# Performance work log

Hardware: AMD Instinct MI355X
Metric: run time of the kernel (lower is better)

Reference implementation:

```python
import jax, jax.numpy as jnp
import numpy as np

C = 256      # d_model
H = 8        # nhead
DF = 1024    # dim_feedforward
LE = 2048    # ego tokens
LA = 2048    # other-agent tokens
N_MATCH = 1024


def setup_inputs() -> dict:
    key = jax.random.key(0)
    ks = jax.random.split(key, 16)
    def rn(k, shape, s=0.02):
        return jax.random.normal(k, shape, dtype=jnp.float32) * s
    inp = {}
    inp['x_ego'] = jax.random.normal(ks[0], (LE, C), dtype=jnp.float32)
    inp['x_agent'] = jax.random.normal(ks[1], (LA, C), dtype=jnp.float32)
    # query_fusion MLP(2C -> C -> C -> C), torch Linear weight is (out, in)
    inp['Wf1'] = rn(ks[2], (C, 2 * C)); inp['bf1'] = jnp.zeros((C,), jnp.float32)
    inp['Wf2'] = rn(ks[3], (C, C));     inp['bf2'] = jnp.zeros((C,), jnp.float32)
    inp['Wf3'] = rn(ks[4], (C, C));     inp['bf3'] = jnp.zeros((C,), jnp.float32)
    # nn.MultiheadAttention packed in-proj and out-proj
    inp['Wqkv'] = rn(ks[5], (3 * C, C)); inp['bqkv'] = jnp.zeros((3 * C,), jnp.float32)
    inp['Wo'] = rn(ks[6], (C, C));       inp['bo'] = jnp.zeros((C,), jnp.float32)
    # FFN
    inp['W1'] = rn(ks[7], (DF, C)); inp['b1'] = jnp.zeros((DF,), jnp.float32)
    inp['W2'] = rn(ks[8], (C, DF)); inp['b2'] = jnp.zeros((C,), jnp.float32)
    # LayerNorms
    inp['g1'] = jnp.ones((C,), jnp.float32); inp['be1'] = jnp.zeros((C,), jnp.float32)
    inp['g2'] = jnp.ones((C,), jnp.float32); inp['be2'] = jnp.zeros((C,), jnp.float32)
    # unique 1D positions: first N_MATCH agent positions overlap ego, rest don't
    inp['pos_ego'] = jnp.arange(LE, dtype=jnp.int32)
    pa = np.concatenate([np.arange(N_MATCH), np.arange(LA - N_MATCH) + 10_000_000])
    inp['pos_agent'] = jnp.asarray(pa, dtype=jnp.int32)
    inp['n_remain'] = LA - N_MATCH  # static python int
    return inp


def _ln(t, g, b):
    m = t.mean(-1, keepdims=True)
    v = t.var(-1, keepdims=True)
    return (t - m) / jnp.sqrt(v + 1e-5) * g + b


def reference(x_ego, x_agent, Wf1, bf1, Wf2, bf2, Wf3, bf3, Wqkv, bqkv, Wo, bo,
              W1, b1, W2, b2, g1, be1, g2, be2, pos_ego, pos_agent, n_remain):
    # ---- position-keyed grouping / fuse (replaces the host-side dict loop) ----
    eq = pos_agent[:, None] == pos_ego[None, :]          # [La, Le]
    matched_e = eq.any(axis=0)                           # ego token has same-pos agent token
    agent_for_ego = jnp.argmax(eq, axis=0)               # [Le] matching agent index (valid where matched)
    fused_in = jnp.concatenate([x_ego, x_agent[agent_for_ego]], axis=-1)  # [Le, 2C]
    h = jax.nn.relu(fused_in @ Wf1.T + bf1)
    h = jax.nn.relu(h @ Wf2.T + bf2)
    fused = h @ Wf3.T + bf3                              # query_fusion MLP output [Le, C]
    ego_out = jnp.where(matched_e[:, None], fused, x_ego)
    # agent tokens with no ego match, in original agent order (fixed count n_remain)
    remain_idx = jnp.nonzero(~eq.any(axis=1), size=n_remain)[0]
    q = jnp.concatenate([ego_out, x_agent[remain_idx]], axis=0)[None]  # (1, Lq, C)
    kv = jnp.concatenate([x_ego, x_agent], axis=0)[None]               # (1, Lk, C)
    # ---- MultiheadAttention (batch_first, eval: dropout off) ----
    Wq, Wk, Wv = jnp.split(Wqkv, 3, axis=0)
    bq, bk, bv = jnp.split(bqkv, 3, axis=0)
    dh = C // H
    def heads(t, W, b):
        return (t @ W.T + b).reshape(1, -1, H, dh).transpose(0, 2, 1, 3)
    qh, kh, vh = heads(q, Wq, bq), heads(kv, Wk, bk), heads(kv, Wv, bv)
    scores = jnp.einsum('bhqd,bhkd->bhqk', qh, kh) / (float(dh) ** 0.5)
    attn = jax.nn.softmax(scores, axis=-1)
    o = jnp.einsum('bhqk,bhkd->bhqd', attn, vh).transpose(0, 2, 1, 3).reshape(1, -1, C)
    o = o @ Wo.T + bo
    # ---- residual + norm1 + FFN + residual + norm2 ----
    yq = _ln(q + o, g1, be1)
    ff = jax.nn.relu(yq @ W1.T + b1) @ W2.T + b2
    return _ln(yq + ff, g2, be2)
```

## Files before the change

kernel.cpp:

```cpp
#include <hip/hip_runtime.h>


#define LE 2048
#define LA 2048
#define CDIM 256
#define HN 8
#define DH 32
#define DFF 1024
#define NREM 1024
#define LQC 3072
#define LKC 4096
#define KSPLIT 8
#define NIT (LKC / KSPLIT / 64)

typedef unsigned short u16;
typedef unsigned int u32;
typedef __attribute__((ext_vector_type(8))) short bf16x8;
typedef __attribute__((ext_vector_type(4))) float f32x4;

__device__ __forceinline__ u32 pk_bf16(float a, float b) {
    u32 ua = (__builtin_bit_cast(u32, a) + 0x8000u) >> 16;
    u32 ub = (__builtin_bit_cast(u32, b) + 0x8000u) >> 16;
    return ua | (ub << 16);
}
__device__ __forceinline__ u16 bf16_1(float a) {
    return (u16)((__builtin_bit_cast(u32, a) + 0x8000u) >> 16);
}
__device__ __forceinline__ float fast_exp2(float x) {
    return __builtin_amdgcn_exp2f(x);
}

__global__ __launch_bounds__(1024) void k_match(const int* __restrict__ pos_ego,
                                                const int* __restrict__ pos_agent,
                                                int* __restrict__ afe,
                                                int* __restrict__ matched,
                                                int* __restrict__ unmatched) {
    __shared__ int keyA[4096], valA[4096], keyE[4096];
    const int t = threadIdx.x;
#pragma unroll
    for (int i = 0; i < 4; ++i) { keyA[t + i * 1024] = -1; keyE[t + i * 1024] = -1; }
    __syncthreads();
#pragma unroll
    for (int i = 0; i < 2; ++i) {
        int a = t + i * 1024;
        int p = pos_agent[a];
        u32 h = ((u32)p * 2654435761u) >> 20;
        while (true) {
            int prev = atomicCAS(&keyA[h], -1, p);
            if (prev == -1) { valA[h] = a; break; }
            h = (h + 1) & 4095;
        }
        int e = t + i * 1024;
        int pe = pos_ego[e];
        u32 he = ((u32)pe * 2654435761u) >> 20;
        while (true) {
            int prev = atomicCAS(&keyE[he], -1, pe);
            if (prev == -1) break;
            he = (he + 1) & 4095;
        }
    }
    __syncthreads();
#pragma unroll
    for (int i = 0; i < 2; ++i) {
        int e = t + i * 1024;
        int p = pos_ego[e];
        u32 h = ((u32)p * 2654435761u) >> 20;
        int idx = 0, fnd = 0;
        while (true) {
            int k = keyA[h];
            if (k == p) { idx = valA[h]; fnd = 1; break; }
            if (k == -1) break;
            h = (h + 1) & 4095;
        }
        afe[e] = idx;
        matched[e] = fnd;
        int a = t + i * 1024;
        int pa_ = pos_agent[a];
        u32 ha = ((u32)pa_ * 2654435761u) >> 20;
        int fnd2 = 0;
        while (true) {
            int k = keyE[ha];
            if (k == pa_) { fnd2 = 1; break; }
            if (k == -1) break;
            ha = (ha + 1) & 4095;
        }
        unmatched[a] = !fnd2;
    }
}

struct WPtrs { const float* p[7]; };
__constant__ __device__ const int woff[8] = {0, 131072, 196608, 262144,
                                             458752, 524288, 786432, 1048576};

__global__ __launch_bounds__(256) void k_stage2(const int* __restrict__ unmatched,
                                                int* __restrict__ remain,
                                                const int* __restrict__ afe,
                                                const float* __restrict__ x_ego,
                                                const float* __restrict__ x_agent,
                                                u16* __restrict__ fused_b,
                                                WPtrs wp, u16* __restrict__ wb,
                                                u16* __restrict__ kv_b) {
    int b = blockIdx.x;
    if (b == 0) {
        __shared__ int s[256];
        int t = threadIdx.x;
        int base_i = t * 8;
        int flags[8];
        int cnt = 0;
#pragma unroll
        for (int j = 0; j < 8; ++j) { flags[j] = unmatched[base_i + j]; cnt += flags[j]; }
        s[t] = cnt;
        __syncthreads();
        for (int off = 1; off < 256; off <<= 1) {
            int v = (t >= off) ? s[t - off] : 0;
            __syncthreads();
            s[t] += v;
            __syncthreads();
        }
        int pos = s[t] - cnt;
#pragma unroll
        for (int j = 0; j < 8; ++j) {
            if (flags[j]) {
                if (pos < NREM) remain[pos] = base_i + j;
                pos++;
            }
        }
    } else if (b <= 512) {
        int t = (b - 1) * 256 + threadIdx.x;
        int e = t >> 6, c8 = t & 63;
        const float* src;
        int col;
        if (c8 < 32) { src = x_ego + (size_t)e * CDIM; col = c8 * 8; }
        else { src = x_agent + (size_t)afe[e] * CDIM; col = (c8 - 32) * 8; }
        float4 f0 = *(const float4*)(src + col);
        float4 f1 = *(const float4*)(src + col + 4);
        uint4 o;
        o.x = pk_bf16(f0.x, f0.y); o.y = pk_bf16(f0.z, f0.w);
        o.z = pk_bf16(f1.x, f1.y); o.w = pk_bf16(f1.z, f1.w);
        *(uint4*)(fused_b + (size_t)e * 512 + c8 * 8) = o;
    } else if (b <= 1024) {
        int g = ((b - 513) * 256 + threadIdx.x) * 8;
        int s = 0;
#pragma unroll
        for (int i = 1; i < 7; ++i) s += (g >= woff[i]);
        const float* src = wp.p[s] + (g - woff[s]);
        float4 f0 = *(const float4*)(src);
        float4 f1 = *(const float4*)(src + 4);
        uint4 o;
        o.x = pk_bf16(f0.x, f0.y); o.y = pk_bf16(f0.z, f0.w);
        o.z = pk_bf16(f1.x, f1.y); o.w = pk_bf16(f1.z, f1.w);
        *(uint4*)(wb + g) = o;
    } else {
        int t = (b - 1025) * 256 + threadIdx.x;
        int j = t >> 5, c8 = t & 31;
        const float* src = (j < LE) ? (x_ego + (size_t)j * CDIM)
                                    : (x_agent + (size_t)(j - LE) * CDIM);
        float4 f0 = *(const float4*)(src + c8 * 8);
        float4 f1 = *(const float4*)(src + c8 * 8 + 4);
        uint4 o;
        o.x = pk_bf16(f0.x, f0.y); o.y = pk_bf16(f0.z, f0.w);
        o.z = pk_bf16(f1.x, f1.y); o.w = pk_bf16(f1.z, f1.w);
        *(uint4*)(kv_b + (size_t)j * CDIM + c8 * 8) = o;
    }
}

__global__ __launch_bounds__(256) void k_finalize_q(const int* __restrict__ matched,
                                                    const int* __restrict__ remain,
                                                    const float* __restrict__ x_ego,
                                                    const float* __restrict__ x_agent,
                                                    float* __restrict__ qbuf,
                                                    u16* __restrict__ qbuf_b) {
    int t = blockIdx.x * 256 + threadIdx.x;
    int row = t >> 5, c8 = t & 31;
    const float* src;
    if (row < LE) {
        src = matched[row] ? (qbuf + (size_t)row * CDIM) : (x_ego + (size_t)row * CDIM);
    } else {
        int idx = remain[row - LE];
        idx = min(max(idx, 0), LA - 1);
        src = x_agent + (size_t)idx * CDIM;
    }
    float4 f0 = *(const float4*)(src + c8 * 8);
    float4 f1 = *(const float4*)(src + c8 * 8 + 4);
    float* dst = qbuf + (size_t)row * CDIM + c8 * 8;
    *(float4*)(dst) = f0;
    *(float4*)(dst + 4) = f1;
    uint4 o;
    o.x = pk_bf16(f0.x, f0.y); o.y = pk_bf16(f0.z, f0.w);
    o.z = pk_bf16(f1.x, f1.y); o.w = pk_bf16(f1.z, f1.w);
    *(uint4*)(qbuf_b + (size_t)row * CDIM + c8 * 8) = o;
}

template <int EPI, bool RELU>
__global__ __launch_bounds__(256) void gemm_bf16(const u16* __restrict__ A,
                                                 const u16* __restrict__ B,
                                                 const float* __restrict__ bias,
                                                 void* __restrict__ C,
                                                 int M, int N, int K) {
    const int tid = threadIdx.x;
    const int w = tid >> 6, lane = tid & 63;
    const int quad = lane >> 4, qi = lane & 15;
    const int wm = w >> 1, wn = w & 1;
    const int bm = blockIdx.y * 64, bn = blockIdx.x * 64;

    const u16* pa0 = A + (size_t)(bm + wm * 32 + qi) * K + quad * 8;
    const u16* pa1 = pa0 + (size_t)16 * K;
    const u16* pb0 = B + (size_t)(bn + wn * 32 + qi) * K + quad * 8;
    const u16* pb1 = pb0 + (size_t)16 * K;

    f32x4 acc00 = {0.f, 0.f, 0.f, 0.f}, acc01 = {0.f, 0.f, 0.f, 0.f};
    f32x4 acc10 = {0.f, 0.f, 0.f, 0.f}, acc11 = {0.f, 0.f, 0.f, 0.f};

#pragma unroll 4
    for (int k = 0; k < K; k += 32) {
        bf16x8 a0 = *(const bf16x8*)(pa0 + k);
        bf16x8 a1 = *(const bf16x8*)(pa1 + k);
        bf16x8 b0 = *(const bf16x8*)(pb0 + k);
        bf16x8 b1 = *(const bf16x8*)(pb1 + k);
        acc00 = __builtin_amdgcn_mfma_f32_16x16x32_bf16(a0, b0, acc00, 0, 0, 0);
        acc01 = __builtin_amdgcn_mfma_f32_16x16x32_bf16(a0, b1, acc01, 0, 0, 0);
        acc10 = __builtin_amdgcn_mfma_f32_16x16x32_bf16(a1, b0, acc10, 0, 0, 0);
        acc11 = __builtin_amdgcn_mfma_f32_16x16x32_bf16(a1, b1, acc11, 0, 0, 0);
    }

#pragma unroll
    for (int i = 0; i < 2; ++i) {
#pragma unroll
        for (int j = 0; j < 2; ++j) {
            f32x4 acc = (i == 0) ? (j == 0 ? acc00 : acc01) : (j == 0 ? acc10 : acc11);
            int n = bn + wn * 32 + j * 16 + qi;
            int mbase = bm + wm * 32 + i * 16 + quad * 4;
            float bs = bias[n];
            float v[4];
#pragma unroll
            for (int r = 0; r < 4; ++r) {
                float x = acc[r] + bs;
                if (RELU) x = fmaxf(x, 0.f);
                v[r] = x;
            }
            if (EPI == 0) {
                float* Cf = (float*)C;
#pragma unroll
                for (int r = 0; r < 4; ++r) Cf[(size_t)(mbase + r) * N + n] = v[r];
            } else {
                u16* Cb = (u16*)C;
#pragma unroll
                for (int r = 0; r < 4; ++r) Cb[(size_t)(mbase + r) * N + n] = bf16_1(v[r]);
            }
        }
    }
}

__global__ __launch_bounds__(256) void k_qkv(const u16* __restrict__ qbuf_b,
                                             const u16* __restrict__ kv_b,
                                             const u16* __restrict__ Wq,
                                             const u16* __restrict__ Wkv,
                                             const float* __restrict__ bqkv,
                                             u16* __restrict__ qb,
                                             u16* __restrict__ kbp,
                                             u16* __restrict__ vtb,
                                             float qscale) {
    int b = blockIdx.x;
    const u16 *A, *B;
    const float* bias;
    int bm, bn, mode;
    if (b < 192) {
        A = qbuf_b; B = Wq; bias = bqkv;
        bm = (b >> 2) * 64; bn = (b & 3) * 64; mode = 0;
    } else {
        int c = b - 192;
        A = kv_b; B = Wkv; bias = bqkv + 256;
        bm = (c >> 3) * 64; bn = (c & 7) * 64; mode = 1;
    }
    const int tid = threadIdx.x;
    const int w = tid >> 6, lane = tid & 63;
    const int quad = lane >> 4, qi = lane & 15;
    const int wm = w >> 1, wn = w & 1;
    const int K = 256;

    const u16* pa0 = A + (size_t)(bm + wm * 32 + qi) * K + quad * 8;
    const u16* pa1 = pa0 + (size_t)16 * K;
    const u16* pb0 = B + (size_t)(bn + wn * 32 + qi) * K + quad * 8;
    const u16* pb1 = pb0 + (size_t)16 * K;

    f32x4 acc00 = {0.f, 0.f, 0.f, 0.f}, acc01 = {0.f, 0.f, 0.f, 0.f};
    f32x4 acc10 = {0.f, 0.f, 0.f, 0.f}, acc11 = {0.f, 0.f, 0.f, 0.f};
#pragma unroll 4
    for (int k = 0; k < 256; k += 32) {
        bf16x8 a0 = *(const bf16x8*)(pa0 + k);
        bf16x8 a1 = *(const bf16x8*)(pa1 + k);
        bf16x8 b0 = *(const bf16x8*)(pb0 + k);
        bf16x8 b1 = *(const bf16x8*)(pb1 + k);
        acc00 = __builtin_amdgcn_mfma_f32_16x16x32_bf16(a0, b0, acc00, 0, 0, 0);
        acc01 = __builtin_amdgcn_mfma_f32_16x16x32_bf16(a0, b1, acc01, 0, 0, 0);
        acc10 = __builtin_amdgcn_mfma_f32_16x16x32_bf16(a1, b0, acc10, 0, 0, 0);
        acc11 = __builtin_amdgcn_mfma_f32_16x16x32_bf16(a1, b1, acc11, 0, 0, 0);
    }
#pragma unroll
    for (int i = 0; i < 2; ++i) {
#pragma unroll
        for (int j = 0; j < 2; ++j) {
            f32x4 acc = (i == 0) ? (j == 0 ? acc00 : acc01) : (j == 0 ? acc10 : acc11);
            int n = bn + wn * 32 + j * 16 + qi;
            int mbase = bm + wm * 32 + i * 16 + quad * 4;
            float bs = bias[n];
            float v[4];
#pragma unroll
            for (int r = 0; r < 4; ++r) v[r] = acc[r] + bs;
            if (mode == 0) {
#pragma unroll
                for (int r = 0; r < 4; ++r)
                    qb[(size_t)(mbase + r) * 256 + n] = bf16_1(v[r] * qscale);
            } else if (n < 256) {
#pragma unroll
                for (int r = 0; r < 4; ++r)
                    kbp[(size_t)(mbase + r) * 256 + n] = bf16_1(v[r]);
            } else {
                ushort4 o4;
                o4.x = bf16_1(v[0]); o4.y = bf16_1(v[1]);
                o4.z = bf16_1(v[2]); o4.w = bf16_1(v[3]);
                *(ushort4*)(vtb + (size_t)(n - 256) * LKC + mbase) = o4;
            }
        }
    }
}

__global__ __launch_bounds__(256) void attn_mfma(const u16* __restrict__ qb,
                                                 const u16* __restrict__ kb,
                                                 const u16* __restrict__ vtb,
                                                 float* __restrict__ Pl,
                                                 float* __restrict__ Pacc) {
    __shared__ u16 Kt[2][64 * 32];
    __shared__ u16 Vt[2][32 * 64];
    __shared__ u16 plds[4][16 * 64];
    const int tid = threadIdx.x;
    const int w = tid >> 6, lane = tid & 63;
    const int quad = lane >> 4, qi = lane & 15;
    const int h = blockIdx.y, ks = blockIdx.z;
    const int q0 = blockIdx.x * 64 + w * 16;

    bf16x8 qf = *(const bf16x8*)(qb + (size_t)(q0 + qi) * CDIM + h * DH + quad * 8);

    f32x4 O0 = {0.f, 0.f, 0.f, 0.f}, O1 = {0.f, 0.f, 0.f, 0.f};
    float lsum = 0.f;

    const int krow = w * 16 + (lane >> 2), kcp = lane & 3;
    const int kc = kcp ^ (krow & 3);
    const u16* kg0 = kb + (size_t)krow * CDIM + h * DH + kc * 8;
    const int kdst = krow * 32 + kcp * 8;
    const int vd = w * 8 + (lane >> 3), vcp = lane & 7;
    const int vc = vcp ^ (vd & 7);
    const u16* vg0 = vtb + (size_t)(h * DH + vd) * LKC + vc * 8;
    const int vdst = vd * 64 + vcp * 8;

    const int ka0 = qi * 32 + ((quad ^ (qi & 3)) << 3);
    const int v00o = qi * 64 + ((quad ^ (qi & 7)) << 3);
    const int v01o = qi * 64 + (((quad + 4) ^ (qi & 7)) << 3);
    const int swz = (qi & 7);
    const int rd0 = qi * 64 + ((quad ^ swz) << 3);
    const int rd1 = qi * 64 + (((4 + quad) ^ swz) << 3);
    const int half = (quad & 1) << 2;

    int kt = ks * (LKC / KSPLIT);
    {
        bf16x8 kr = *(const bf16x8*)(kg0 + (size_t)kt * CDIM);
        bf16x8 vr = *(const bf16x8*)(vg0 + kt);
        *(bf16x8*)&Kt[0][kdst] = kr;
        *(bf16x8*)&Vt[0][vdst] = vr;
    }
    int buf = 0;
    for (int it = 0; it < NIT; ++it, kt += 64) {
        __syncthreads();
        bf16x8 knext, vnext;
        const bool more = (it + 1 < NIT);
        if (more) {
            knext = *(const bf16x8*)(kg0 + (size_t)(kt + 64) * CDIM);
            vnext = *(const bf16x8*)(vg0 + kt + 64);
        }

        bf16x8 a0 = *(const bf16x8*)&Kt[buf][ka0];
        bf16x8 a1 = *(const bf16x8*)&Kt[buf][ka0 + 16 * 32];
        bf16x8 a2 = *(const bf16x8*)&Kt[buf][ka0 + 32 * 32];
        bf16x8 a3 = *(const bf16x8*)&Kt[buf][ka0 + 48 * 32];
        f32x4 z = {0.f, 0.f, 0.f, 0.f};
        f32x4 s0 = __builtin_amdgcn_mfma_f32_16x16x32_bf16(a0, qf, z, 0, 0, 0);
        f32x4 s1 = __builtin_amdgcn_mfma_f32_16x16x32_bf16(a1, qf, z, 0, 0, 0);
        f32x4 s2 = __builtin_amdgcn_mfma_f32_16x16x32_bf16(a2, qf, z, 0, 0, 0);
        f32x4 s3 = __builtin_amdgcn_mfma_f32_16x16x32_bf16(a3, qf, z, 0, 0, 0);

        float p0[4], p1[4], p2[4], p3[4];
#pragma unroll
        for (int r = 0; r < 4; ++r) {
            p0[r] = fast_exp2(s0[r]); p1[r] = fast_exp2(s1[r]);
            p2[r] = fast_exp2(s2[r]); p3[r] = fast_exp2(s3[r]);
            lsum += p0[r] + p1[r] + p2[r] + p3[r];
        }

        u16* pb = &plds[w][0];
#pragma unroll
        for (int t2 = 0; t2 < 4; ++t2) {
            int jg = t2 * 2 + (quad >> 1);
            int off = qi * 64 + ((jg ^ swz) << 3) + half;
            uint2 pw;
            float* pp = (t2 == 0) ? p0 : (t2 == 1) ? p1 : (t2 == 2) ? p2 : p3;
            pw.x = pk_bf16(pp[0], pp[1]);
            pw.y = pk_bf16(pp[2], pp[3]);
            *(uint2*)&pb[off] = pw;
        }
        bf16x8 pa0 = *(bf16x8*)&pb[rd0];
        bf16x8 pa1 = *(bf16x8*)&pb[rd1];

        bf16x8 v00 = *(const bf16x8*)&Vt[buf][v00o];
        bf16x8 v01 = *(const bf16x8*)&Vt[buf][v01o];
        bf16x8 v10 = *(const bf16x8*)&Vt[buf][v00o + 16 * 64];
        bf16x8 v11 = *(const bf16x8*)&Vt[buf][v01o + 16 * 64];
        O0 = __builtin_amdgcn_mfma_f32_16x16x32_bf16(pa0, v00, O0, 0, 0, 0);
        O0 = __builtin_amdgcn_mfma_f32_16x16x32_bf16(pa1, v01, O0, 0, 0, 0);
        O1 = __builtin_amdgcn_mfma_f32_16x16x32_bf16(pa0, v10, O1, 0, 0, 0);
        O1 = __builtin_amdgcn_mfma_f32_16x16x32_bf16(pa1, v11, O1, 0, 0, 0);

        if (more) {
            *(bf16x8*)&Kt[buf ^ 1][kdst] = knext;
            *(bf16x8*)&Vt[buf ^ 1][vdst] = vnext;
        }
        buf ^= 1;
    }

    lsum += __shfl_xor(lsum, 16, 64);
    lsum += __shfl_xor(lsum, 32, 64);

    int pbase = (h * KSPLIT + ks) * LQC + q0;
    if (quad == 0) Pl[pbase + qi] = lsum;
#pragma unroll
    for (int r = 0; r < 4; ++r) {
        int q = quad * 4 + r;
        float* pa = Pacc + (size_t)(pbase + q) * 32;
        pa[qi] = O0[r];
        pa[16 + qi] = O1[r];
    }
}

__global__ __launch_bounds__(256) void attn_combine(const float* __restrict__ Pl,
                                                    const float* __restrict__ Pacc,
                                                    u16* __restrict__ attn_b) {
    int t = blockIdx.x * 256 + threadIdx.x;
    int row = t >> 6;
    int h = (t >> 3) & 7;
    int d4 = t & 7;
    float L = 0.f;
    float o[4] = {};
#pragma unroll
    for (int ck = 0; ck < KSPLIT; ++ck) {
        size_t pidx = (size_t)(h * KSPLIT + ck) * LQC + row;
        L += Pl[pidx];
        float4 a = *(const float4*)(Pacc + pidx * 32 + d4 * 4);
        o[0] += a.x; o[1] += a.y; o[2] += a.z; o[3] += a.w;
    }
    float inv = 1.0f / L;
    ushort4 ov;
    ov.x = bf16_1(o[0] * inv); ov.y = bf16_1(o[1] * inv);
    ov.z = bf16_1(o[2] * inv); ov.w = bf16_1(o[3] * inv);
    *(ushort4*)(attn_b + (size_t)row * CDIM + h * DH + d4 * 4) = ov;
}

template <bool EMIT_BF16>
__global__ __launch_bounds__(256) void ln_kernel(const float* __restrict__ X,
                                                 const float* __restrict__ R,
                                                 const float* __restrict__ g,
                                                 const float* __restrict__ b,
                                                 float* __restrict__ out,
                                                 u16* __restrict__ out_b) {
    int lane = threadIdx.x & 63;
    int row = blockIdx.x * 4 + (threadIdx.x >> 6);
    const float* x = X + (size_t)row * CDIM;
    const float* r = R + (size_t)row * CDIM;
    float4 xv = *(const float4*)(x + lane * 4);
    float4 rv = *(const float4*)(r + lane * 4);
    float v[4] = {xv.x + rv.x, xv.y + rv.y, xv.z + rv.z, xv.w + rv.w};
    float s = v[0] + v[1] + v[2] + v[3];
    float sq = v[0] * v[0] + v[1] * v[1] + v[2] * v[2] + v[3] * v[3];
#pragma unroll
    for (int off = 32; off >= 1; off >>= 1) {
        s += __shfl_xor(s, off, 64);
        sq += __shfl_xor(sq, off, 64);
    }
    float mean = s * (1.f / 256.f);
    float var = sq * (1.f / 256.f) - mean * mean;
    float rstd = rsqrtf(var + 1e-5f);
    float4 gv = *(const float4*)(g + lane * 4);
    float4 bv = *(const float4*)(b + lane * 4);
    float4 o = make_float4((v[0] - mean) * rstd * gv.x + bv.x,
                           (v[1] - mean) * rstd * gv.y + bv.y,
                           (v[2] - mean) * rstd * gv.z + bv.z,
                           (v[3] - mean) * rstd * gv.w + bv.w);
    *(float4*)(out + (size_t)row * CDIM + lane * 4) = o;
    if (EMIT_BF16) {
        uint2 ob;
        ob.x = pk_bf16(o.x, o.y);
        ob.y = pk_bf16(o.z, o.w);
        *(uint2*)(out_b + (size_t)row * CDIM + lane * 4) = ob;
    }
}

extern "C" void kernel_launch(void* const* d_in, const int* in_sizes, int n_in,
                              void* d_out, int out_size, void* d_ws, size_t ws_size,
                              hipStream_t stream) {
    const float* x_ego = (const float*)d_in[0];
    const float* x_agent = (const float*)d_in[1];
    const float* Wf1 = (const float*)d_in[2];
    const float* bf1 = (const float*)d_in[3];
    const float* Wf2 = (const float*)d_in[4];
    const float* bf2 = (const float*)d_in[5];
    const float* Wf3 = (const float*)d_in[6];
    const float* bf3 = (const float*)d_in[7];
    const float* Wqkv = (const float*)d_in[8];
    const float* bqkv = (const float*)d_in[9];
    const float* Wo = (const float*)d_in[10];
    const float* bo = (const float*)d_in[11];
    const float* W1 = (const float*)d_in[12];
    const float* b1 = (const float*)d_in[13];
    const float* W2 = (const float*)d_in[14];
    const float* b2 = (const float*)d_in[15];
    const float* g1 = (const float*)d_in[16];
    const float* be1 = (const float*)d_in[17];
    const float* g2 = (const float*)d_in[18];
    const float* be2 = (const float*)d_in[19];
    const int* pos_ego = (const int*)d_in[20];
    const int* pos_agent = (const int*)d_in[21];

    float* ws = (float*)d_ws;
    size_t o = 0;
    float* qbuf = ws + o; o += 786432;
    float* o2 = ws + o; o += 786432;
    float* yq = ws + o; o += 786432;
    float* ff2 = o2;
    float* Pl = ws + o; o += HN * KSPLIT * LQC;
    float* Pacc = ws + o; o += (size_t)HN * KSPLIT * LQC * 32;
    u16* wb = (u16*)(ws + o); o += 524288;
    u16* fused_b = (u16*)(ws + o); o += 524288;
    u16* h1_b = (u16*)(ws + o); o += 262144;
    u16* h2_b = (u16*)(ws + o); o += 262144;
    u16* qbuf_b = (u16*)(ws + o); o += 393216;
    u16* kv_b = (u16*)(ws + o); o += 524288;
    u16* qb = (u16*)(ws + o); o += 393216;
    u16* kb = (u16*)(ws + o); o += 524288;
    u16* vtb = (u16*)(ws + o); o += 524288;
    u16* attn_b = (u16*)(ws + o); o += 393216;
    u16* ff1_b = (u16*)(ws + o); o += 1572864;
    u16* yq_b = (u16*)(ws + o); o += 393216;
    int* afe = (int*)(ws + o);
    int* matched = afe + LE;
    int* unmatched = matched + LE;
    int* remain = unmatched + LA;

    const u16* Wf1_b = wb + 0;
    const u16* Wf2_b = wb + 131072;
    const u16* Wf3_b = wb + 196608;
    const u16* Wq_b = wb + 262144;
    const u16* Wkv_b = wb + 327680;
    const u16* Wo_b = wb + 458752;
    const u16* W1_b = wb + 524288;
    const u16* W2_b = wb + 786432;

    k_match<<<1, 1024, 0, stream>>>(pos_ego, pos_agent, afe, matched, unmatched);
    WPtrs wp;
    wp.p[0] = Wf1; wp.p[1] = Wf2; wp.p[2] = Wf3; wp.p[3] = Wqkv;
    wp.p[4] = Wo; wp.p[5] = W1; wp.p[6] = W2;
    k_stage2<<<1537, 256, 0, stream>>>(unmatched, remain, afe, x_ego, x_agent,
                                       fused_b, wp, wb, kv_b);

    const float qscale = 0.17677669529663687f * 1.4426950408889634f;

    gemm_bf16<1, true><<<dim3(4, 32), 256, 0, stream>>>(fused_b, Wf1_b, bf1, h1_b,
                                                        LE, 256, 512);
    gemm_bf16<1, true><<<dim3(4, 32), 256, 0, stream>>>(h1_b, Wf2_b, bf2, h2_b,
                                                        LE, 256, 256);
    gemm_bf16<0, false><<<dim3(4, 32), 256, 0, stream>>>(h2_b, Wf3_b, bf3, qbuf,
                                                         LE, 256, 256);
    k_finalize_q<<<(LQC * 32) / 256, 256, 0, stream>>>(matched, remain, x_ego, x_agent,
                                                       qbuf, qbuf_b);

    k_qkv<<<704, 256, 0, stream>>>(qbuf_b, kv_b, Wq_b, Wkv_b, bqkv, qb, kb, vtb, qscale);

    attn_mfma<<<dim3(LQC / 64, HN, KSPLIT), 256, 0, stream>>>(qb, kb, vtb, Pl, Pacc);
    attn_combine<<<(LQC * 64) / 256, 256, 0, stream>>>(Pl, Pacc, attn_b);

    gemm_bf16<0, false><<<dim3(4, 48), 256, 0, stream>>>(attn_b, Wo_b, bo, o2,
                                                         LQC, 256, 256);
    ln_kernel<true><<<LQC / 4, 256, 0, stream>>>(qbuf, o2, g1, be1, yq, yq_b);

    gemm_bf16<1, true><<<dim3(16, 48), 256, 0, stream>>>(yq_b, W1_b, b1, ff1_b,
                                                         LQC, DFF, 256);
    gemm_bf16<0, false><<<dim3(4, 48), 256, 0, stream>>>(ff1_b, W2_b, b2, ff2,
                                                         LQC, 256, DFF);
    ln_kernel<false><<<LQC / 4, 256, 0, stream>>>(yq, ff2, g2, be2, (float*)d_out, nullptr);
}
```

Baseline: 218.6 us.

## Fuse attention combine, out-proj and LayerNorms; fold q finalize into MLP GEMM

Three kernel fusions cut launch count and intermediate global traffic. The last query-fusion GEMM now also does the matched/unmatched select and the gather of remaining agent rows, replacing k_finalize_q. The split-K attention combine, Wo projection, residual add and LayerNorm1 become one kernel over 16-row tiles using LDS. The W2 GEMM is fused with residual add and LayerNorm2. Each fused GEMM tile covers the full 256-column width over only 16 rows, which gives fewer blocks (192) and reloads weights per block, so occupancy and reuse may be lower.

Measured after the change: 231.4 us. 5.8% more time.

```diff
diff --git a/kernel.cpp b/kernel.cpp
--- a/kernel.cpp
+++ b/kernel.cpp
@@ -164,33 +164,6 @@
     }
 }
 
-__global__ __launch_bounds__(256) void k_finalize_q(const int* __restrict__ matched,
-                                                    const int* __restrict__ remain,
-                                                    const float* __restrict__ x_ego,
-                                                    const float* __restrict__ x_agent,
-                                                    float* __restrict__ qbuf,
-                                                    u16* __restrict__ qbuf_b) {
-    int t = blockIdx.x * 256 + threadIdx.x;
-    int row = t >> 5, c8 = t & 31;
-    const float* src;
-    if (row < LE) {
-        src = matched[row] ? (qbuf + (size_t)row * CDIM) : (x_ego + (size_t)row * CDIM);
-    } else {
-        int idx = remain[row - LE];
-        idx = min(max(idx, 0), LA - 1);
-        src = x_agent + (size_t)idx * CDIM;
-    }
-    float4 f0 = *(const float4*)(src + c8 * 8);
-    float4 f1 = *(const float4*)(src + c8 * 8 + 4);
-    float* dst = qbuf + (size_t)row * CDIM + c8 * 8;
-    *(float4*)(dst) = f0;
-    *(float4*)(dst + 4) = f1;
-    uint4 o;
-    o.x = pk_bf16(f0.x, f0.y); o.y = pk_bf16(f0.z, f0.w);
-    o.z = pk_bf16(f1.x, f1.y); o.w = pk_bf16(f1.z, f1.w);
-    *(uint4*)(qbuf_b + (size_t)row * CDIM + c8 * 8) = o;
-}
-
 template <int EPI, bool RELU>
 __global__ __launch_bounds__(256) void gemm_bf16(const u16* __restrict__ A,
                                                  const u16* __restrict__ B,
@@ -249,6 +222,71 @@
             }
         }
     }
+}
+
+__global__ __launch_bounds__(256) void k_mlp3f(const u16* __restrict__ h2_b,
+                                               const u16* __restrict__ Wf3_b,
+                                               const float* __restrict__ bf3,
+                                               const int* __restrict__ matched,
+                                               const int* __restrict__ remain,
+                                               const float* __restrict__ x_ego,
+                                               const float* __restrict__ x_agent,
+                                               float* __restrict__ qbuf,
+                                               u16* __restrict__ qbuf_b) {
+    const int tid = threadIdx.x;
+    const int bn = blockIdx.x * 64, bm = blockIdx.y * 64;
+    if (bm >= LE) {
+        int row = bm + (tid >> 2);
+        int col = bn + (tid & 3) * 16;
+        int idx = remain[row - LE];
+        idx = min(max(idx, 0), LA - 1);
+        const float* src = x_agent + (size_t)idx * CDIM + col;
+        float* dq = qbuf + (size_t)row * CDIM + col;
+        u16* db = qbuf_b + (size_t)row * CDIM + col;
+#pragma unroll
+        for (int i = 0; i < 4; ++i) {
+            float4 v = *(const float4*)(src + i * 4);
+            *(float4*)(dq + i * 4) = v;
+            *(uint2*)(db + i * 4) = make_uint2(pk_bf16(v.x, v.y), pk_bf16(v.z, v.w));
+        }
+        return;
+    }
+    const int w = tid >> 6, lane = tid & 63;
+    const int quad = lane >> 4, qi = lane & 15;
+    const int wm = w >> 1, wn = w & 1;
+    const u16* pa0 = h2_b + (size_t)(bm + wm * 32 + qi) * 256 + quad * 8;
+    const u16* pa1 = pa0 + (size_t)16 * 256;
+    const u16* pb0 = Wf3_b + (size_t)(bn + wn * 32 + qi) * 256 + quad * 8;
+    const u16* pb1 = pb0 + (size_t)16 * 256;
+    f32x4 a00 = {0, 0, 0, 0}, a01 = {0, 0, 0, 0}, a10 = {0, 0, 0, 0}, a11 = {0, 0, 0, 0};
+#pragma unroll 4
+    for (int k = 0; k < 256; k += 32) {
+        bf16x8 x0 = *(const bf16x8*)(pa0 + k);
+        bf16x8 x1 = *(const bf16x8*)(pa1 + k);
+        bf16x8 y0 = *(const bf16x8*)(pb0 + k);
+        bf16x8 y1 = *(const bf16x8*)(pb1 + k);
+        a00 = __builtin_amdgcn_mfma_f32_16x16x32_bf16(x0, y0, a00, 0, 0, 0);
+        a01 = __builtin_amdgcn_mfma_f32_16x16x32_bf16(x0, y1, a01, 0, 0, 0);
+        a10 = __builtin_amdgcn_mfma_f32_16x16x32_bf16(x1, y0, a10, 0, 0, 0);
+        a11 = __builtin_amdgcn_mfma_f32_16x16x32_bf16(x1, y1, a11, 0, 0, 0);
+    }
+#pragma unroll
+    for (int i = 0; i < 2; ++i)
+#pragma unroll
+        for (int jj = 0; jj < 2; ++jj) {
+            f32x4 acc = (i == 0) ? (jj == 0 ? a00 : a01) : (jj == 0 ? a10 : a11);
+            int n = bn + wn * 32 + jj * 16 + qi;
+            int mb = bm + wm * 32 + i * 16 + quad * 4;
+            float bs = bf3[n];
+#pragma unroll
+            for (int r = 0; r < 4; ++r) {
+                int row = mb + r;
+                float v = acc[r] + bs;
+                if (!matched[row]) v = x_ego[(size_t)row * CDIM + n];
+                qbuf[(size_t)row * CDIM + n] = v;
+                qbuf_b[(size_t)row * CDIM + n] = bf16_1(v);
+            }
+        }
 }
 
 __global__ __launch_bounds__(256) void k_qkv(const u16* __restrict__ qbuf_b,
@@ -440,65 +478,159 @@
     }
 }
 
-__global__ __launch_bounds__(256) void attn_combine(const float* __restrict__ Pl,
-                                                    const float* __restrict__ Pacc,
-                                                    u16* __restrict__ attn_b) {
-    int t = blockIdx.x * 256 + threadIdx.x;
-    int row = t >> 6;
-    int h = (t >> 3) & 7;
-    int d4 = t & 7;
-    float L = 0.f;
-    float o[4] = {};
-#pragma unroll
-    for (int ck = 0; ck < KSPLIT; ++ck) {
-        size_t pidx = (size_t)(h * KSPLIT + ck) * LQC + row;
-        L += Pl[pidx];
-        float4 a = *(const float4*)(Pacc + pidx * 32 + d4 * 4);
-        o[0] += a.x; o[1] += a.y; o[2] += a.z; o[3] += a.w;
-    }
-    float inv = 1.0f / L;
-    ushort4 ov;
-    ov.x = bf16_1(o[0] * inv); ov.y = bf16_1(o[1] * inv);
-    ov.z = bf16_1(o[2] * inv); ov.w = bf16_1(o[3] * inv);
-    *(ushort4*)(attn_b + (size_t)row * CDIM + h * DH + d4 * 4) = ov;
-}
-
-template <bool EMIT_BF16>
-__global__ __launch_bounds__(256) void ln_kernel(const float* __restrict__ X,
-                                                 const float* __restrict__ R,
-                                                 const float* __restrict__ g,
-                                                 const float* __restrict__ b,
-                                                 float* __restrict__ out,
-                                                 u16* __restrict__ out_b) {
-    int lane = threadIdx.x & 63;
-    int row = blockIdx.x * 4 + (threadIdx.x >> 6);
-    const float* x = X + (size_t)row * CDIM;
-    const float* r = R + (size_t)row * CDIM;
-    float4 xv = *(const float4*)(x + lane * 4);
-    float4 rv = *(const float4*)(r + lane * 4);
-    float v[4] = {xv.x + rv.x, xv.y + rv.y, xv.z + rv.z, xv.w + rv.w};
-    float s = v[0] + v[1] + v[2] + v[3];
-    float sq = v[0] * v[0] + v[1] * v[1] + v[2] * v[2] + v[3] * v[3];
-#pragma unroll
-    for (int off = 32; off >= 1; off >>= 1) {
-        s += __shfl_xor(s, off, 64);
-        sq += __shfl_xor(sq, off, 64);
-    }
-    float mean = s * (1.f / 256.f);
-    float var = sq * (1.f / 256.f) - mean * mean;
-    float rstd = rsqrtf(var + 1e-5f);
-    float4 gv = *(const float4*)(g + lane * 4);
-    float4 bv = *(const float4*)(b + lane * 4);
-    float4 o = make_float4((v[0] - mean) * rstd * gv.x + bv.x,
-                           (v[1] - mean) * rstd * gv.y + bv.y,
-                           (v[2] - mean) * rstd * gv.z + bv.z,
-                           (v[3] - mean) * rstd * gv.w + bv.w);
-    *(float4*)(out + (size_t)row * CDIM + lane * 4) = o;
-    if (EMIT_BF16) {
+__global__ __launch_bounds__(256) void k_oln(const float* __restrict__ Pl,
+                                             const float* __restrict__ Pacc,
+                                             const u16* __restrict__ Wo_b,
+                                             const float* __restrict__ bo,
+                                             const float* __restrict__ qbuf,
+                                             const float* __restrict__ g1,
+                                             const float* __restrict__ be1,
+                                             float* __restrict__ yq,
+                                             u16* __restrict__ yq_b) {
+    __shared__ u16 Alds[16][264];
+    __shared__ float olds[16][260];
+    const int tid = threadIdx.x;
+    const int r0 = blockIdx.x * 16;
+    {
+        int rl = tid >> 4, tc = tid & 15;
+        int row = r0 + rl;
+        int h = tc >> 1;
+        int sub = (tc & 1) * 16;
+        float L = 0.f;
+        float acc[16] = {};
+#pragma unroll
+        for (int ck = 0; ck < KSPLIT; ++ck) {
+            size_t pidx = (size_t)(h * KSPLIT + ck) * LQC + row;
+            L += Pl[pidx];
+            const float* pa = Pacc + pidx * 32 + sub;
+#pragma unroll
+            for (int i = 0; i < 4; ++i) {
+                float4 v = *(const float4*)(pa + i * 4);
+                acc[i * 4 + 0] += v.x; acc[i * 4 + 1] += v.y;
+                acc[i * 4 + 2] += v.z; acc[i * 4 + 3] += v.w;
+            }
+        }
+        float inv = 1.f / L;
+        u32* dst = (u32*)&Alds[rl][tc * 16];
+#pragma unroll
+        for (int i = 0; i < 8; ++i)
+            dst[i] = pk_bf16(acc[2 * i] * inv, acc[2 * i + 1] * inv);
+    }
+    __syncthreads();
+    const int w = tid >> 6, lane = tid & 63;
+    const int quad = lane >> 4, qi = lane & 15;
+    f32x4 accs[4] = {{0, 0, 0, 0}, {0, 0, 0, 0}, {0, 0, 0, 0}, {0, 0, 0, 0}};
+    const u16* pb = Wo_b + (size_t)(w * 64 + qi) * 256 + quad * 8;
+#pragma unroll
+    for (int ks = 0; ks < 8; ++ks) {
+        bf16x8 af = *(const bf16x8*)&Alds[qi][ks * 32 + quad * 8];
+#pragma unroll
+        for (int j = 0; j < 4; ++j) {
+            bf16x8 bf = *(const bf16x8*)(pb + (size_t)j * 16 * 256 + ks * 32);
+            accs[j] = __builtin_amdgcn_mfma_f32_16x16x32_bf16(af, bf, accs[j], 0, 0, 0);
+        }
+    }
+#pragma unroll
+    for (int j = 0; j < 4; ++j) {
+        int n = w * 64 + j * 16 + qi;
+        float bs = bo[n];
+#pragma unroll
+        for (int r = 0; r < 4; ++r) olds[quad * 4 + r][n] = accs[j][r] + bs;
+    }
+    __syncthreads();
+#pragma unroll
+    for (int rr = 0; rr < 4; ++rr) {
+        int rl = w * 4 + rr;
+        int row = r0 + rl;
+        float4 rv = *(const float4*)(qbuf + (size_t)row * CDIM + lane * 4);
+        float v[4];
+        v[0] = olds[rl][lane * 4 + 0] + rv.x;
+        v[1] = olds[rl][lane * 4 + 1] + rv.y;
+        v[2] = olds[rl][lane * 4 + 2] + rv.z;
+        v[3] = olds[rl][lane * 4 + 3] + rv.w;
+        float s = v[0] + v[1] + v[2] + v[3];
+        float sq = v[0] * v[0] + v[1] * v[1] + v[2] * v[2] + v[3] * v[3];
+#pragma unroll
+        for (int off = 32; off >= 1; off >>= 1) {
+            s += __shfl_xor(s, off, 64);
+            sq += __shfl_xor(sq, off, 64);
+        }
+        float mean = s * (1.f / 256.f);
+        float var = sq * (1.f / 256.f) - mean * mean;
+        float rstd = rsqrtf(var + 1e-5f);
+        float4 gv = *(const float4*)(g1 + lane * 4);
+        float4 bv = *(const float4*)(be1 + lane * 4);
+        float o0 = (v[0] - mean) * rstd * gv.x + bv.x;
+        float o1 = (v[1] - mean) * rstd * gv.y + bv.y;
+        float o2 = (v[2] - mean) * rstd * gv.z + bv.z;
+        float o3 = (v[3] - mean) * rstd * gv.w + bv.w;
+        *(float4*)(yq + (size_t)row * CDIM + lane * 4) = make_float4(o0, o1, o2, o3);
         uint2 ob;
-        ob.x = pk_bf16(o.x, o.y);
-        ob.y = pk_bf16(o.z, o.w);
-        *(uint2*)(out_b + (size_t)row * CDIM + lane * 4) = ob;
+        ob.x = pk_bf16(o0, o1);
+        ob.y = pk_bf16(o2, o3);
+        *(uint2*)(yq_b + (size_t)row * CDIM + lane * 4) = ob;
+    }
+}
+
+__global__ __launch_bounds__(256) void k_f2ln(const u16* __restrict__ ff1_b,
+                                              const u16* __restrict__ W2_b,
+                                              const float* __restrict__ b2,
+                                              const float* __restrict__ yq,
+                                              const float* __restrict__ g2,
+                                              const float* __restrict__ be2,
+                                              float* __restrict__ out) {
+    __shared__ float olds[16][260];
+    const int tid = threadIdx.x;
+    const int r0 = blockIdx.x * 16;
+    const int w = tid >> 6, lane = tid & 63;
+    const int quad = lane >> 4, qi = lane & 15;
+    const u16* pa = ff1_b + (size_t)(r0 + qi) * DFF + quad * 8;
+    const u16* pb = W2_b + (size_t)(w * 64 + qi) * DFF + quad * 8;
+    f32x4 accs[4] = {{0, 0, 0, 0}, {0, 0, 0, 0}, {0, 0, 0, 0}, {0, 0, 0, 0}};
+#pragma unroll 4
+    for (int ks = 0; ks < 32; ++ks) {
+        bf16x8 af = *(const bf16x8*)(pa + ks * 32);
+#pragma unroll
+        for (int j = 0; j < 4; ++j) {
+            bf16x8 bf = *(const bf16x8*)(pb + (size_t)j * 16 * DFF + ks * 32);
+            accs[j] = __builtin_amdgcn_mfma_f32_16x16x32_bf16(af, bf, accs[j], 0, 0, 0);
+        }
+    }
+#pragma unroll
+    for (int j = 0; j < 4; ++j) {
+        int n = w * 64 + j * 16 + qi;
+        float bs = b2[n];
+#pragma unroll
+        for (int r = 0; r < 4; ++r) olds[quad * 4 + r][n] = accs[j][r] + bs;
+    }
+    __syncthreads();
+#pragma unroll
+    for (int rr = 0; rr < 4; ++rr) {
+        int rl = w * 4 + rr;
+        int row = r0 + rl;
+        float4 rv = *(const float4*)(yq + (size_t)row * CDIM + lane * 4);
+        float v[4];
+        v[0] = olds[rl][lane * 4 + 0] + rv.x;
+        v[1] = olds[rl][lane * 4 + 1] + rv.y;
+        v[2] = olds[rl][lane * 4 + 2] + rv.z;
+        v[3] = olds[rl][lane * 4 + 3] + rv.w;
+        float s = v[0] + v[1] + v[2] + v[3];
+        float sq = v[0] * v[0] + v[1] * v[1] + v[2] * v[2] + v[3] * v[3];
+#pragma unroll
+        for (int off = 32; off >= 1; off >>= 1) {
+            s += __shfl_xor(s, off, 64);
+            sq += __shfl_xor(sq, off, 64);
+        }
+        float mean = s * (1.f / 256.f);
+        float var = sq * (1.f / 256.f) - mean * mean;
+        float rstd = rsqrtf(var + 1e-5f);
+        float4 gv = *(const float4*)(g2 + lane * 4);
+        float4 bv = *(const float4*)(be2 + lane * 4);
+        float4 o = make_float4((v[0] - mean) * rstd * gv.x + bv.x,
+                               (v[1] - mean) * rstd * gv.y + bv.y,
+                               (v[2] - mean) * rstd * gv.z + bv.z,
+                               (v[3] - mean) * rstd * gv.w + bv.w);
+        *(float4*)(out + (size_t)row * CDIM + lane * 4) = o;
     }
 }
 
@@ -531,9 +663,7 @@
     float* ws = (float*)d_ws;
     size_t o = 0;
     float* qbuf = ws + o; o += 786432;
-    float* o2 = ws + o; o += 786432;
     float* yq = ws + o; o += 786432;
-    float* ff2 = o2;
     float* Pl = ws + o; o += HN * KSPLIT * LQC;
     float* Pacc = ws + o; o += (size_t)HN * KSPLIT * LQC * 32;
     u16* wb = (u16*)(ws + o); o += 524288;
@@ -545,7 +675,6 @@
     u16* qb = (u16*)(ws + o); o += 393216;
     u16* kb = (u16*)(ws + o); o += 524288;
     u16* vtb = (u16*)(ws + o); o += 524288;
-    u16* attn_b = (u16*)(ws + o); o += 393216;
     u16* ff1_b = (u16*)(ws + o); o += 1572864;
     u16* yq_b = (u16*)(ws + o); o += 393216;
     int* afe = (int*)(ws + o);
@@ -575,23 +704,16 @@
                                                         LE, 256, 512);
     gemm_bf16<1, true><<<dim3(4, 32), 256, 0, stream>>>(h1_b, Wf2_b, bf2, h2_b,
                                                         LE, 256, 256);
-    gemm_bf16<0, false><<<dim3(4, 32), 256, 0, stream>>>(h2_b, Wf3_b, bf3, qbuf,
-                                                         LE, 256, 256);
-    k_finalize_q<<<(LQC * 32) / 256, 256, 0, stream>>>(matched, remain, x_ego, x_agent,
-                                                       qbuf, qbuf_b);
+    k_mlp3f<<<dim3(4, 48), 256, 0, stream>>>(h2_b, Wf3_b, bf3, matched, remain,
+                                             x_ego, x_agent, qbuf, qbuf_b);
 
     k_qkv<<<704, 256, 0, stream>>>(qbuf_b, kv_b, Wq_b, Wkv_b, bqkv, qb, kb, vtb, qscale);
 
     attn_mfma<<<dim3(LQC / 64, HN, KSPLIT), 256, 0, stream>>>(qb, kb, vtb, Pl, Pacc);
-    attn_combine<<<(LQC * 64) / 256, 256, 0, stream>>>(Pl, Pacc, attn_b);
-
-    gemm_bf16<0, false><<<dim3(4, 48), 256, 0, stream>>>(attn_b, Wo_b, bo, o2,
-                                                         LQC, 256, 256);
-    ln_kernel<true><<<LQC / 4, 256, 0, stream>>>(qbuf, o2, g1, be1, yq, yq_b);
+
+    k_oln<<<LQC / 16, 256, 0, stream>>>(Pl, Pacc, Wo_b, bo, qbuf, g1, be1, yq, yq_b);
 
     gemm_bf16<1, true><<<dim3(16, 48), 256, 0, stream>>>(yq_b, W1_b, b1, ff1_b,
                                                          LQC, DFF, 256);
-    gemm_bf16<0, false><<<dim3(4, 48), 256, 0, stream>>>(ff1_b, W2_b, b2, ff2,
-                                                         LQC, 256, DFF);
-    ln_kernel<false><<<LQC / 4, 256, 0, stream>>>(yq, ff2, g2, be2, (float*)d_out, nullptr);
-}
+    k_f2ln<<<LQC / 16, 256, 0, stream>>>(ff1_b, W2_b, b2, yq, g2, be2, (float*)d_out);
+}
```
